# Kernel tuning notes

Measured on AMD Instinct MI355X. Metric: run time of the kernel, lower is better.

## Reference

```python
import jax, jax.numpy as jnp
import numpy as np

B, S, C, D = 128, 128, 128, 64
NQ, NT = 5000, 1441

def setup_inputs() -> dict:
    key = jax.random.key(0)
    ks = jax.random.split(key, 20)
    def xav(k, shape):
        fan_in, fan_out = shape[0], shape[1]
        lim = float(np.sqrt(6.0 / (fan_in + fan_out)))
        return jax.random.uniform(k, shape, jnp.float32, -lim, lim)
    return {
        'question_seq': jax.random.randint(ks[0], (B, S), 0, NQ),
        'correctness_seq': jax.random.randint(ks[1], (B, S), 0, 2),
        'interval_time_seq': jax.random.randint(ks[2], (B, S), 0, NT),
        'use_time_seq': jax.random.randint(ks[3], (B, S), 0, NT),
        'E_q': jax.random.normal(ks[4], (NQ, D), jnp.float32) * 0.05,
        'E_c': jax.random.normal(ks[5], (2, D), jnp.float32) * 0.05,
        'E_it': jax.random.normal(ks[6], (NT, D), jnp.float32) * 0.05,
        'E_at': jax.random.normal(ks[7], (NT, D), jnp.float32) * 0.05,
        'q_matrix': (jax.random.uniform(ks[8], (NQ, C)) < 0.1).astype(jnp.float32),
        'h0': xav(ks[9], (C, D)),
        'W1': xav(ks[10], (3 * D, D)), 'b1': jnp.zeros((D,), jnp.float32),
        'W2': xav(ks[11], (4 * D, D)), 'b2': jnp.zeros((D,), jnp.float32),
        'W3': xav(ks[12], (4 * D, D)), 'b3': jnp.zeros((D,), jnp.float32),
        'W4': xav(ks[13], (3 * D, D)), 'b4': jnp.zeros((D,), jnp.float32),
        'W5': xav(ks[14], (2 * D, D)), 'b5': jnp.zeros((D,), jnp.float32),
    }

def _lpkt_forward(question_seq, correctness_seq, interval_time_seq, use_time_seq,
                  E_q, E_c, E_it, E_at, q_matrix, h0,
                  W1, b1, W2, b2, W3, b3, W4, b4, W5, b5):
    dim_k = W1.shape[1]
    b, s = question_seq.shape
    e_emb = E_q[question_seq]            # [B,S,D]
    c_emb = E_c[correctness_seq]         # [B,S,D]
    it_emb = E_it[interval_time_seq]     # [B,S,D]
    at_emb = E_at[use_time_seq]          # [B,S,D]
    # all learning vectors (linear_1 over full sequence, as in original)
    all_learning = jnp.concatenate([e_emb, at_emb, c_emb], -1) @ W1 + b1  # [B,S,D]
    q_e_seq = q_matrix[question_seq]     # [B,S,C]

    h_pre0 = jnp.broadcast_to(h0, (b,) + h0.shape)                 # [B,C,D]
    h_tilde0 = q_e_seq[:, 0] @ h0                                  # [B,D] (h_pre is batch-replicated)
    learning0 = jnp.zeros((b, dim_k), all_learning.dtype)

    # time-major xs for t = 0 .. s-2
    xs = (jnp.swapaxes(q_e_seq[:, :-1], 0, 1),      # q_e at t
          jnp.swapaxes(q_e_seq[:, 1:], 0, 1),       # q_e at t+1
          jnp.swapaxes(it_emb[:, :-1], 0, 1),       # it at t
          jnp.swapaxes(all_learning[:, :-1], 0, 1), # learning at t
          jnp.swapaxes(e_emb[:, 1:], 0, 1))         # e embed at t+1

    def step(carry, x):
        h_pre, h_tilde_pre, learning_pre = carry
        q_e, q_e_next, it, learning, e_next = x
        x4 = jnp.concatenate([learning_pre, it, learning, h_tilde_pre], -1)   # [B,4D]
        learning_gain = jnp.tanh(x4 @ W2 + b2)
        gamma_l = jax.nn.sigmoid(x4 @ W3 + b3)
        LG = gamma_l * (learning_gain + 1.0) * 0.5                            # [B,D]
        LG_tilde = q_e[:, :, None] * LG[:, None, :]                           # [B,C,D] scatter to concepts
        c = q_e.shape[1]
        x3 = jnp.concatenate([h_pre,
                              jnp.broadcast_to(LG[:, None, :], (LG.shape[0], c, dim_k)),
                              jnp.broadcast_to(it[:, None, :], (it.shape[0], c, dim_k))], -1)
        gamma_f = jax.nn.sigmoid(x3 @ W4 + b4)                                # [B,C,D]
        h = LG_tilde + gamma_f * h_pre                                        # [B,C,D]
        h_tilde = jnp.einsum('bc,bcd->bd', q_e_next, h)                       # gather for next question
        y = jax.nn.sigmoid(jnp.concatenate([e_next, h_tilde], -1) @ W5 + b5).mean(-1)
        return (h, h_tilde, learning), y

    _, ys = jax.lax.scan(step, (h_pre0, h_tilde0, learning0), xs)  # ys: [S-1, B]
    pred = jnp.zeros((b, s), ys.dtype).at[:, 1:].set(jnp.swapaxes(ys, 0, 1))
    return pred

def reference(question_seq, correctness_seq, interval_time_seq, use_time_seq,
              E_q, E_c, E_it, E_at, q_matrix, h0,
              W1, b1, W2, b2, W3, b3, W4, b4, W5, b5):
    return _lpkt_forward(question_seq, correctness_seq, interval_time_seq, use_time_seq,
                         E_q, E_c, E_it, E_at, q_matrix, h0,
                         W1, b1, W2, b2, W3, b3, W4, b4, W5, b5)
```

## Files before the change

kernel.cpp:

```cpp
#include <hip/hip_runtime.h>
#include <hip/hip_bf16.h>


#define NB 128
#define NS 128
#define NC 128
#define ND 64
#define POS (NB*NS)

typedef __attribute__((ext_vector_type(8))) short short8;
typedef __attribute__((ext_vector_type(4))) float f32x4;
typedef __attribute__((ext_vector_type(2))) _Float16 half2_t;

__device__ __forceinline__ float rl(float v,int j){
  return __int_as_float(__builtin_amdgcn_readlane(__float_as_int(v), j));
}
__device__ __forceinline__ half2_t rlh2(half2_t v,int j){
  int x; __builtin_memcpy(&x,&v,4);
  x = __builtin_amdgcn_readlane(x,j);
  half2_t r; __builtin_memcpy(&r,&x,4); return r;
}
__device__ __forceinline__ half2_t pkrtz(float a, float b){
  auto t = __builtin_amdgcn_cvt_pkrtz(a,b);
  half2_t r; __builtin_memcpy(&r,&t,4); return r;
}
__device__ __forceinline__ float dppswap(float v){
  return __int_as_float(__builtin_amdgcn_update_dpp(0,__float_as_int(v),0xB1,0xF,0xF,true));
}
__device__ __forceinline__ float dot2h(half2_t a, half2_t b, float c){
#if __has_builtin(__builtin_amdgcn_fdot2)
  return __builtin_amdgcn_fdot2(a,b,c,false);
#else
  return fmaf((float)a[0],(float)b[0], fmaf((float)a[1],(float)b[1], c));
#endif
}

#define HBF(c, d) ((((c)<<6) + (d)) ^ (((c)&7)<<3))
#define DPP_ADD(v, CTRL) ((v) + __int_as_float(__builtin_amdgcn_update_dpp(0, __float_as_int(v), CTRL, 0xF, 0xF, true)))
#define DPP_ROWSUM(v) do { v = DPP_ADD(v,0x111); v = DPP_ADD(v,0x112); v = DPP_ADD(v,0x114); v = DPP_ADD(v,0x118); } while(0)

#define SC1 (-1.4426950408889634f)

__device__ __forceinline__ float gsig(float zp){
  return __builtin_amdgcn_rcpf(1.f + __builtin_amdgcn_exp2f(zp));
}

__global__ __launch_bounds__(64) void lpkt_pre1(
    const int* __restrict__ qseq, const int* __restrict__ cseq,
    const int* __restrict__ itseq, const int* __restrict__ atseq,
    const float* __restrict__ E_q, const float* __restrict__ E_c,
    const float* __restrict__ E_it, const float* __restrict__ E_at,
    const float* __restrict__ W1, const float* __restrict__ b1,
    const float* __restrict__ W4, const float* __restrict__ b4,
    const float* __restrict__ W5, const float* __restrict__ b5,
    float* __restrict__ AL, float* __restrict__ pre4, float* __restrict__ pre5)
{
  __shared__ float sx[4][192];
  __shared__ float sit[4][64];
  const int d = threadIdx.x;
  #pragma unroll
  for (int i = 0; i < 4; ++i) {
    int p = blockIdx.x + i*4096;
    sx[i][d]      = E_q[qseq[p]*ND + d];
    sx[i][64+d]   = E_at[atseq[p]*ND + d];
    sx[i][128+d]  = E_c[cseq[p]*ND + d];
    sit[i][d]     = E_it[itseq[p]*ND + d];
  }
  __syncthreads();
  float al[4], p4[4], p5[4];
  const float b1d = b1[d], b4d = b4[d], b5d = b5[d];
  #pragma unroll
  for (int i = 0; i < 4; ++i) { al[i] = b1d; p4[i] = b4d; p5[i] = b5d; }
  for (int k = 0; k < 192; ++k) {
    float wv = W1[k*ND + d];
    #pragma unroll
    for (int i = 0; i < 4; ++i) al[i] = fmaf(sx[i][k], wv, al[i]);
  }
  for (int k = 0; k < 64; ++k) {
    float wv4 = W4[(128+k)*ND + d];
    float wv5 = W5[k*ND + d];
    #pragma unroll
    for (int i = 0; i < 4; ++i) {
      p4[i] = fmaf(sit[i][k], wv4, p4[i]);
      p5[i] = fmaf(sx[i][k],  wv5, p5[i]);
    }
  }
  #pragma unroll
  for (int i = 0; i < 4; ++i) {
    int p = blockIdx.x + i*4096;
    AL[p*ND + d]   = al[i];
    pre4[p*ND + d] = p4[i]*SC1;
    pre5[p*ND + d] = p5[i]*SC1;
  }
}

__global__ __launch_bounds__(64) void lpkt_pre2(
    const int* __restrict__ itseq, const float* __restrict__ E_it,
    const float* __restrict__ AL,
    const float* __restrict__ W2, const float* __restrict__ b2,
    const float* __restrict__ W3, const float* __restrict__ b3,
    float* __restrict__ pre2, float* __restrict__ pre3)
{
  __shared__ float sx[4][192];
  const int d = threadIdx.x;
  int bs4[4];
  #pragma unroll
  for (int i = 0; i < 4; ++i) {
    int p = blockIdx.x + i*4064;
    int b = p / 127;
    int t = p - b*127;
    int bs = b*NS + t;
    bs4[i] = bs;
    sx[i][d]     = (t > 0) ? AL[(bs-1)*ND + d] : 0.f;
    sx[i][64+d]  = E_it[itseq[bs]*ND + d];
    sx[i][128+d] = AL[bs*ND + d];
  }
  __syncthreads();
  float a2[4], a3[4];
  const float b2d = b2[d], b3d = b3[d];
  #pragma unroll
  for (int i = 0; i < 4; ++i) { a2[i] = b2d; a3[i] = b3d; }
  for (int k = 0; k < 192; ++k) {
    float w2v = W2[k*ND + d];
    float w3v = W3[k*ND + d];
    #pragma unroll
    for (int i = 0; i < 4; ++i) {
      a2[i] = fmaf(sx[i][k], w2v, a2[i]);
      a3[i] = fmaf(sx[i][k], w3v, a3[i]);
    }
  }
  #pragma unroll
  for (int i = 0; i < 4; ++i) {
    pre2[bs4[i]*ND + d] = a2[i]*(2.f*SC1);
    pre3[bs4[i]*ND + d] = a3[i]*SC1;
  }
}

#define LOADB() do {                                                         \
  _Pragma("unroll")                                                          \
  for (int t2_=0;t2_<2;++t2_)                                                \
    _Pragma("unroll")                                                        \
    for (int k0_=0;k0_<2;++k0_)                                              \
      bfr[t2_][k0_] = *(const short8*)&sh_hbf[bfofs[t2_][k0_]];              \
} while(0)

#define MFMA8() do {                                                         \
  _Pragma("unroll")                                                          \
  for (int t2_=0;t2_<2;++t2_){                                               \
    _Pragma("unroll")                                                        \
    for (int k0_=0;k0_<2;++k0_){                                             \
      acc[0][t2_] = __builtin_amdgcn_mfma_f32_16x16x32_bf16(aW[0][k0_], bfr[t2_][k0_], acc[0][t2_],0,0,0); \
      acc[1][t2_] = __builtin_amdgcn_mfma_f32_16x16x32_bf16(aW[1][k0_], bfr[t2_][k0_], acc[1][t2_],0,0,0); \
    }                                                                        \
  }                                                                          \
} while(0)

__global__ __launch_bounds__(512)
void lpkt_seq(
    const int* __restrict__ qseq, const float* __restrict__ qmat,
    const float* __restrict__ h0,
    const float* __restrict__ W2, const float* __restrict__ W3,
    const float* __restrict__ W4, const float* __restrict__ W5,
    const float* __restrict__ pre2, const float* __restrict__ pre3,
    const float* __restrict__ pre4, const float* __restrict__ pre5,
    float* __restrict__ out)
{
  __shared__ __align__(16) unsigned short sh_hbf[NC*ND];
  __shared__ float sh_pre[32][4][64];
  __shared__ float sh_qf[32][NC];
  __shared__ float sh_htp[4][64];
  __shared__ float sh_LG[64];
  __shared__ __align__(16) unsigned sh_LGb[32];
  __shared__ float sh_out[NS];

  const int tid = threadIdx.x;
  const int w = tid>>6, l = tid&63;
  const int g = l>>4, li = l&15;
  const int b = blockIdx.x;
  const int Wq = w & 3, mm = (w>>2)*2;

  if (w==4) __builtin_amdgcn_s_setprio(1);

  short8 aW[2][2];
  #pragma unroll
  for (int mloc=0;mloc<2;++mloc)
    #pragma unroll
    for (int k0=0;k0<2;++k0){
      short8 v;
      #pragma unroll
      for (int j=0;j<8;++j){
        __hip_bfloat16 hb = __float2bfloat16(W4[(32*k0+8*g+j)*ND + 16*(mm+mloc)+li] * SC1);
        v[j] = *(short*)&hb;
      }
      aW[mloc][k0] = v;
    }
  short8 aW4b[2][2];
  #pragma unroll
  for (int mloc=0;mloc<2;++mloc)
    #pragma unroll
    for (int k0=0;k0<2;++k0){
      short8 v;
      #pragma unroll
      for (int j=0;j<8;++j){
        __hip_bfloat16 hb = __float2bfloat16(W4[(64+32*k0+8*g+j)*ND + 16*(mm+mloc)+li] * SC1);
        v[j] = *(short*)&hb;
      }
      aW4b[mloc][k0] = v;
    }

  half2_t wA[32], wB[32];
  if (w==4){
    #pragma unroll
    for (int j=0;j<32;++j){
      wA[j] = pkrtz(W2[(192+2*j)*ND + l]*(2.f*SC1), W2[(193+2*j)*ND + l]*(2.f*SC1));
      wB[j] = pkrtz(W3[(192+2*j)*ND + l]*SC1,       W3[(193+2*j)*ND + l]*SC1);
    }
  } else if (w==6){
    #pragma unroll
    for (int j=0;j<32;++j)
      wA[j] = pkrtz(W5[(64+2*j)*ND + l]*SC1, W5[(65+2*j)*ND + l]*SC1);
  }

  float hreg[2][2][4];
  int wofs[2][2], bfofs[2][2];
  #pragma unroll
  for (int mloc=0;mloc<2;++mloc)
    #pragma unroll
    for (int t2=0;t2<2;++t2){
      int c  = 32*Wq + 16*t2 + li;
      int d0 = 16*(mm+mloc) + 4*g;
      wofs[t2][mloc] = HBF(c, d0);
      float4 v = *(const float4*)&h0[c*ND + d0];
      hreg[mloc][t2][0]=v.x; hreg[mloc][t2][1]=v.y;
      hreg[mloc][t2][2]=v.z; hreg[mloc][t2][3]=v.w;
      __hip_bfloat162 c01 = __float22bfloat162_rn(make_float2(v.x,v.y));
      __hip_bfloat162 c23 = __float22bfloat162_rn(make_float2(v.z,v.w));
      uint2 pk; pk.x = *(unsigned*)&c01; pk.y = *(unsigned*)&c23;
      *(uint2*)&sh_hbf[wofs[t2][mloc]] = pk;
    }
  #pragma unroll
  for (int t2=0;t2<2;++t2)
    #pragma unroll
    for (int k0=0;k0<2;++k0)
      bfofs[t2][k0] = HBF(32*Wq+16*t2+li, 32*k0+8*g);

  #pragma unroll
  for (int k2=0;k2<2;++k2){
    int f4id = tid + k2*512;
    if (f4id < 17*32){
      int r = f4id >> 5, c4 = (f4id & 31)*4;
      int qrow = qseq[b*NS + r];
      float4 v = *(const float4*)&qmat[qrow*NC + c4];
      *(float4*)&sh_qf[r][c4] = v;
    }
  }
  #pragma unroll
  for (int k2=0;k2<2;++k2){
    int f4id = tid + k2*512;
    int u = f4id >> 6;
    int inner = f4id & 63;
    int s = inner >> 4, c4 = (inner & 15)*4;
    const float* ps = (s==0)?pre2:(s==1)?pre3:(s==2)?pre4:pre5;
    float4 v = *(const float4*)&ps[(size_t)(b*NS+u)*ND + c4];
    *(float4*)(&sh_pre[u][0][0] + inner*4) = v;
  }
  if (tid==0) sh_out[0] = 0.f;
  __syncthreads();

  {
    float part[2][4] = {{0.f,0.f,0.f,0.f},{0.f,0.f,0.f,0.f}};
    #pragma unroll
    for (int t2=0;t2<2;++t2){
      float qv = sh_qf[0][32*Wq+16*t2+li];
      #pragma unroll
      for (int mloc=0;mloc<2;++mloc)
        #pragma unroll
        for (int r2=0;r2<4;++r2)
          part[mloc][r2] = fmaf(qv, hreg[mloc][t2][r2], part[mloc][r2]);
    }
    #pragma unroll
    for (int mloc=0;mloc<2;++mloc)
      #pragma unroll
      for (int r2=0;r2<4;++r2){ float v=part[mloc][r2]; DPP_ROWSUM(v); part[mloc][r2]=v; }
    if (li==15){
      #pragma unroll
      for (int mloc=0;mloc<2;++mloc){
        float4 pv; pv.x=part[mloc][0]; pv.y=part[mloc][1]; pv.z=part[mloc][2]; pv.w=part[mloc][3];
        *(float4*)&sh_htp[Wq][16*(mm+mloc)+4*g] = pv;
      }
    }
  }
  __syncthreads();

  float qc0 = sh_qf[0][32*Wq+li];
  float qc1 = sh_qf[0][32*Wq+16+li];

  const float* prebase;
  { int s = l>>4;
    const float* ps = (s==0)?pre2:(s==1)?pre3:(s==2)?pre4:pre5;
    prebase = ps + (size_t)(b*NS)*ND + (l&15)*4; }

  for (int t=0; t<127; ++t){
    const int slot = t & 31, sn = (t+1) & 31;

    f32x4 acc[2][2];
    #pragma unroll
    for (int mloc=0;mloc<2;++mloc)
      #pragma unroll
      for (int t2=0;t2<2;++t2)
        acc[mloc][t2] = (f32x4){0.f,0.f,0.f,0.f};
    short8 bfr[2][2];

    if (w==4){
      float pv2 = sh_pre[slot][0][l], pv3 = sh_pre[slot][1][l];
      float htv = (sh_htp[0][l]+sh_htp[1][l])+(sh_htp[2][l]+sh_htp[3][l]);
      half2_t hpk = pkrtz(htv, dppswap(htv));
      float a20=pv2, a21=0.f, a30=pv3, a31=0.f;
      #pragma unroll
      for (int j=0;j<32;j+=2){
        half2_t ha = rlh2(hpk, 2*j), hb = rlh2(hpk, 2*j+2);
        a20 = dot2h(ha, wA[j],   a20); a21 = dot2h(hb, wA[j+1], a21);
        a30 = dot2h(ha, wB[j],   a30); a31 = dot2h(hb, wB[j+1], a31);
      }
      float LGl = gsig(a30+a31) * gsig(a20+a21);
      sh_LG[l] = LGl;
      float nb = dppswap(LGl);
      if (!(l&1)){
        __hip_bfloat162 pk = __float22bfloat162_rn(make_float2(LGl, nb));
        sh_LGb[l>>1] = *(unsigned*)&pk;
      }
      LOADB(); MFMA8();
    } else if (w==6){
      if (t > 0){
        float pv5 = sh_pre[slot][3][l];
        float htv = (sh_htp[0][l]+sh_htp[1][l])+(sh_htp[2][l]+sh_htp[3][l]);
        half2_t hpk = pkrtz(htv, dppswap(htv));
        float z0 = pv5, z1 = 0.f;
        #pragma unroll
        for (int j=0;j<32;j+=2){
          z0 = dot2h(rlh2(hpk, 2*j),   wA[j],   z0);
          z1 = dot2h(rlh2(hpk, 2*j+2), wA[j+1], z1);
        }
        float yv = gsig(z0+z1);
        DPP_ROWSUM(yv);
        float s = (rl(yv,15)+rl(yv,31))+(rl(yv,47)+rl(yv,63));
        if (l==0) sh_out[t] = s*(1.f/64.f);
      }
      LOADB(); MFMA8();
    } else if (w==3){
      if ((t&15)==0){
        int t0r = t+17;
        #pragma unroll
        for (int rep=0; rep<8; ++rep){
          int f4id = rep*64 + l;
          int r = t0r + (f4id>>5);
          int c4 = (f4id & 31)*4;
          if (r < NS){
            int qrow = qseq[b*NS + r];
            float4 v = *(const float4*)&qmat[qrow*NC + c4];
            *(float4*)&sh_qf[r&31][c4] = v;
          }
        }
      }
      LOADB(); MFMA8();
    } else if (w==7){
      if ((t&15)==0){
        #pragma unroll
        for (int rep=0; rep<16; ++rep){
          int u = t+16+rep;
          if (u < NS){
            float4 v = *(const float4*)&prebase[(size_t)u*ND];
            *(float4*)(&sh_pre[u&31][0][0] + l*4) = v;
          }
        }
      }
      LOADB(); MFMA8();
    } else {
      LOADB(); MFMA8();
    }
    float qn0 = sh_qf[sn][32*Wq+li];
    float qn1 = sh_qf[sn][32*Wq+16+li];
    __syncthreads();

    {
      short8 lgb[2];
      #pragma unroll
      for (int k0=0;k0<2;++k0)
        lgb[k0] = *(const short8*)((const char*)sh_LGb + 64*k0 + 16*g);
      #pragma unroll
      for (int mloc=0;mloc<2;++mloc)
        #pragma unroll
        for (int t2=0;t2<2;++t2){
          acc[mloc][t2] = __builtin_amdgcn_mfma_f32_16x16x32_bf16(aW4b[mloc][0], lgb[0], acc[mloc][t2],0,0,0);
          acc[mloc][t2] = __builtin_amdgcn_mfma_f32_16x16x32_bf16(aW4b[mloc][1], lgb[1], acc[mloc][t2],0,0,0);
        }

      float4 LG4[2]; float gi[2][4];
      #pragma unroll
      for (int mloc=0;mloc<2;++mloc){
        int d0 = 16*(mm+mloc)+4*g;
        LG4[mloc] = *(const float4*)&sh_LG[d0];
        float4 p4v = *(const float4*)&sh_pre[slot][2][d0];
        gi[mloc][0]=p4v.x; gi[mloc][1]=p4v.y; gi[mloc][2]=p4v.z; gi[mloc][3]=p4v.w;
      }
      float part[2][4] = {{0.f,0.f,0.f,0.f},{0.f,0.f,0.f,0.f}};
      #pragma unroll
      for (int t2=0;t2<2;++t2){
        float qcv = t2 ? qc1 : qc0;
        float qnv = t2 ? qn1 : qn0;
        #pragma unroll
        for (int mloc=0;mloc<2;++mloc){
          float lg4a[4] = {LG4[mloc].x, LG4[mloc].y, LG4[mloc].z, LG4[mloc].w};
          float hn[4];
          #pragma unroll
          for (int r2=0;r2<4;++r2){
            float gam = gsig(acc[mloc][t2][r2] + gi[mloc][r2]);
            hn[r2] = fmaf(qcv, lg4a[r2], gam*hreg[mloc][t2][r2]);
            hreg[mloc][t2][r2] = hn[r2];
            part[mloc][r2] = fmaf(qnv, hn[r2], part[mloc][r2]);
          }
          __hip_bfloat162 c01 = __float22bfloat162_rn(make_float2(hn[0],hn[1]));
          __hip_bfloat162 c23 = __float22bfloat162_rn(make_float2(hn[2],hn[3]));
          uint2 pk; pk.x=*(unsigned*)&c01; pk.y=*(unsigned*)&c23;
          *(uint2*)&sh_hbf[wofs[t2][mloc]] = pk;
        }
      }
      #pragma unroll
      for (int mloc=0;mloc<2;++mloc)
        #pragma unroll
        for (int r2=0;r2<4;++r2){ float v=part[mloc][r2]; DPP_ROWSUM(v); part[mloc][r2]=v; }
      if (li==15){
        #pragma unroll
        for (int mloc=0;mloc<2;++mloc){
          float4 pv; pv.x=part[mloc][0]; pv.y=part[mloc][1]; pv.z=part[mloc][2]; pv.w=part[mloc][3];
          *(float4*)&sh_htp[Wq][16*(mm+mloc)+4*g] = pv;
        }
      }
      qc0 = qn0; qc1 = qn1;
    }
    __syncthreads();
  }

  if (w==6){
    float htv = (sh_htp[0][l]+sh_htp[1][l])+(sh_htp[2][l]+sh_htp[3][l]);
    half2_t hpk = pkrtz(htv, dppswap(htv));
    float z0 = sh_pre[31][3][l], z1 = 0.f;
    #pragma unroll
    for (int j=0;j<32;j+=2){
      z0 = dot2h(rlh2(hpk, 2*j),   wA[j],   z0);
      z1 = dot2h(rlh2(hpk, 2*j+2), wA[j+1], z1);
    }
    float yv = gsig(z0+z1);
    DPP_ROWSUM(yv);
    float s = (rl(yv,15)+rl(yv,31))+(rl(yv,47)+rl(yv,63));
    if (l==0) sh_out[127] = s*(1.f/64.f);
  }
  __syncthreads();
  if (tid < NS) out[b*NS + tid] = sh_out[tid];
}

extern "C" void kernel_launch(void* const* d_in, const int* in_sizes, int n_in,
                              void* d_out, int out_size, void* d_ws, size_t ws_size,
                              hipStream_t stream)
{
  const int*   qseq  = (const int*)d_in[0];
  const int*   cseq  = (const int*)d_in[1];
  const int*   itseq = (const int*)d_in[2];
  const int*   atseq = (const int*)d_in[3];
  const float* E_q   = (const float*)d_in[4];
  const float* E_c   = (const float*)d_in[5];
  const float* E_it  = (const float*)d_in[6];
  const float* E_at  = (const float*)d_in[7];
  const float* qmat  = (const float*)d_in[8];
  const float* h0    = (const float*)d_in[9];
  const float* W1    = (const float*)d_in[10];
  const float* b1    = (const float*)d_in[11];
  const float* W2    = (const float*)d_in[12];
  const float* b2    = (const float*)d_in[13];
  const float* W3    = (const float*)d_in[14];
  const float* b3    = (const float*)d_in[15];
  const float* W4    = (const float*)d_in[16];
  const float* b4    = (const float*)d_in[17];
  const float* W5    = (const float*)d_in[18];
  const float* b5    = (const float*)d_in[19];
  float* out = (float*)d_out;

  float* wsf  = (float*)d_ws;
  float* AL   = wsf;
  float* pre2 = wsf + 1*POS*ND;
  float* pre3 = wsf + 2*POS*ND;
  float* pre4 = wsf + 3*POS*ND;
  float* pre5 = wsf + 4*POS*ND;

  lpkt_pre1<<<4096, 64, 0, stream>>>(qseq, cseq, itseq, atseq,
                                     E_q, E_c, E_it, E_at,
                                     W1, b1, W4, b4, W5, b5,
                                     AL, pre4, pre5);
  lpkt_pre2<<<4064, 64, 0, stream>>>(itseq, E_it, AL, W2, b2, W3, b3, pre2, pre3);
  lpkt_seq<<<128, 512, 0, stream>>>(qseq, qmat, h0, W2, W3, W4, W5,
                                    pre2, pre3, pre4, pre5, out);
}
```

Baseline: 273.0 us.

## Batch 16 positions per block in precompute kernels and fold gate bias into MFMA

```diff
diff --git a/kernel.cpp b/kernel.cpp
--- a/kernel.cpp
+++ b/kernel.cpp
@@ -23,6 +23,11 @@
 __device__ __forceinline__ half2_t pkrtz(float a, float b){
   auto t = __builtin_amdgcn_cvt_pkrtz(a,b);
   half2_t r; __builtin_memcpy(&r,&t,4); return r;
+}
+__device__ __forceinline__ unsigned pk_bf16(float lo, float hi){
+  unsigned r;
+  asm("v_cvt_pk_bf16_f32 %0, %1, %2" : "=v"(r) : "v"(lo), "v"(hi));
+  return r;
 }
 __device__ __forceinline__ float dppswap(float v){
   return __int_as_float(__builtin_amdgcn_update_dpp(0,__float_as_int(v),0xB1,0xF,0xF,true));
@@ -55,39 +60,40 @@
     const float* __restrict__ W5, const float* __restrict__ b5,
     float* __restrict__ AL, float* __restrict__ pre4, float* __restrict__ pre5)
 {
-  __shared__ float sx[4][192];
-  __shared__ float sit[4][64];
+  __shared__ float sx[16][192];
+  __shared__ float sit[16][64];
   const int d = threadIdx.x;
-  #pragma unroll
-  for (int i = 0; i < 4; ++i) {
-    int p = blockIdx.x + i*4096;
+  const int base = blockIdx.x * 16;
+  #pragma unroll 4
+  for (int i = 0; i < 16; ++i) {
+    int p = base + i;
     sx[i][d]      = E_q[qseq[p]*ND + d];
     sx[i][64+d]   = E_at[atseq[p]*ND + d];
     sx[i][128+d]  = E_c[cseq[p]*ND + d];
     sit[i][d]     = E_it[itseq[p]*ND + d];
   }
   __syncthreads();
-  float al[4], p4[4], p5[4];
+  float al[16], p4[16], p5[16];
   const float b1d = b1[d], b4d = b4[d], b5d = b5[d];
   #pragma unroll
-  for (int i = 0; i < 4; ++i) { al[i] = b1d; p4[i] = b4d; p5[i] = b5d; }
+  for (int i = 0; i < 16; ++i) { al[i] = b1d; p4[i] = b4d; p5[i] = b5d; }
   for (int k = 0; k < 192; ++k) {
     float wv = W1[k*ND + d];
     #pragma unroll
-    for (int i = 0; i < 4; ++i) al[i] = fmaf(sx[i][k], wv, al[i]);
+    for (int i = 0; i < 16; ++i) al[i] = fmaf(sx[i][k], wv, al[i]);
   }
   for (int k = 0; k < 64; ++k) {
     float wv4 = W4[(128+k)*ND + d];
     float wv5 = W5[k*ND + d];
     #pragma unroll
-    for (int i = 0; i < 4; ++i) {
+    for (int i = 0; i < 16; ++i) {
       p4[i] = fmaf(sit[i][k], wv4, p4[i]);
       p5[i] = fmaf(sx[i][k],  wv5, p5[i]);
     }
   }
   #pragma unroll
-  for (int i = 0; i < 4; ++i) {
-    int p = blockIdx.x + i*4096;
+  for (int i = 0; i < 16; ++i) {
+    int p = base + i;
     AL[p*ND + d]   = al[i];
     pre4[p*ND + d] = p4[i]*SC1;
     pre5[p*ND + d] = p5[i]*SC1;
@@ -101,38 +107,54 @@
     const float* __restrict__ W3, const float* __restrict__ b3,
     float* __restrict__ pre2, float* __restrict__ pre3)
 {
-  __shared__ float sx[4][192];
+  __shared__ float sal[17][64];
+  __shared__ float sit[16][64];
   const int d = threadIdx.x;
-  int bs4[4];
-  #pragma unroll
-  for (int i = 0; i < 4; ++i) {
-    int p = blockIdx.x + i*4064;
-    int b = p / 127;
-    int t = p - b*127;
-    int bs = b*NS + t;
-    bs4[i] = bs;
-    sx[i][d]     = (t > 0) ? AL[(bs-1)*ND + d] : 0.f;
-    sx[i][64+d]  = E_it[itseq[bs]*ND + d];
-    sx[i][128+d] = AL[bs*ND + d];
+  const int b = blockIdx.x >> 3;
+  const int t0 = (blockIdx.x & 7) * 16;
+  #pragma unroll 4
+  for (int i = 0; i < 17; ++i) {
+    int tt = t0 - 1 + i;
+    sal[i][d] = (tt >= 0) ? AL[(b*NS + tt)*ND + d] : 0.f;
+  }
+  #pragma unroll 4
+  for (int i = 0; i < 16; ++i) {
+    sit[i][d] = E_it[itseq[b*NS + t0 + i]*ND + d];
   }
   __syncthreads();
-  float a2[4], a3[4];
+  float a2[16], a3[16];
   const float b2d = b2[d], b3d = b3[d];
   #pragma unroll
-  for (int i = 0; i < 4; ++i) { a2[i] = b2d; a3[i] = b3d; }
-  for (int k = 0; k < 192; ++k) {
-    float w2v = W2[k*ND + d];
-    float w3v = W3[k*ND + d];
-    #pragma unroll
-    for (int i = 0; i < 4; ++i) {
-      a2[i] = fmaf(sx[i][k], w2v, a2[i]);
-      a3[i] = fmaf(sx[i][k], w3v, a3[i]);
-    }
-  }
-  #pragma unroll
-  for (int i = 0; i < 4; ++i) {
-    pre2[bs4[i]*ND + d] = a2[i]*(2.f*SC1);
-    pre3[bs4[i]*ND + d] = a3[i]*SC1;
+  for (int i = 0; i < 16; ++i) { a2[i] = b2d; a3[i] = b3d; }
+  for (int k = 0; k < 64; ++k) {
+    float w2v = W2[k*ND + d], w3v = W3[k*ND + d];
+    #pragma unroll
+    for (int i = 0; i < 16; ++i) {
+      a2[i] = fmaf(sal[i][k], w2v, a2[i]);
+      a3[i] = fmaf(sal[i][k], w3v, a3[i]);
+    }
+  }
+  for (int k = 0; k < 64; ++k) {
+    float w2v = W2[(64+k)*ND + d], w3v = W3[(64+k)*ND + d];
+    #pragma unroll
+    for (int i = 0; i < 16; ++i) {
+      a2[i] = fmaf(sit[i][k], w2v, a2[i]);
+      a3[i] = fmaf(sit[i][k], w3v, a3[i]);
+    }
+  }
+  for (int k = 0; k < 64; ++k) {
+    float w2v = W2[(128+k)*ND + d], w3v = W3[(128+k)*ND + d];
+    #pragma unroll
+    for (int i = 0; i < 16; ++i) {
+      a2[i] = fmaf(sal[i+1][k], w2v, a2[i]);
+      a3[i] = fmaf(sal[i+1][k], w3v, a3[i]);
+    }
+  }
+  #pragma unroll
+  for (int i = 0; i < 16; ++i) {
+    int p = (b*NS + t0 + i)*ND + d;
+    pre2[p] = a2[i]*(2.f*SC1);
+    pre3[p] = a3[i]*SC1;
   }
 }
 
@@ -153,6 +175,14 @@
       acc[1][t2_] = __builtin_amdgcn_mfma_f32_16x16x32_bf16(aW[1][k0_], bfr[t2_][k0_], acc[1][t2_],0,0,0); \
     }                                                                        \
   }                                                                          \
+} while(0)
+
+#define ACCINIT() do {                                                       \
+  float4 p4a_ = *(const float4*)&sh_pre[slot][2][16*mm+4*g];                 \
+  float4 p4b_ = *(const float4*)&sh_pre[slot][2][16*(mm+1)+4*g];             \
+  f32x4 ia_ = (f32x4){p4a_.x,p4a_.y,p4a_.z,p4a_.w};                          \
+  f32x4 ib_ = (f32x4){p4b_.x,p4b_.y,p4b_.z,p4b_.w};                          \
+  acc[0][0]=ia_; acc[0][1]=ia_; acc[1][0]=ib_; acc[1][1]=ib_;                \
 } while(0)
 
 __global__ __launch_bounds__(512)
@@ -233,9 +263,7 @@
       float4 v = *(const float4*)&h0[c*ND + d0];
       hreg[mloc][t2][0]=v.x; hreg[mloc][t2][1]=v.y;
       hreg[mloc][t2][2]=v.z; hreg[mloc][t2][3]=v.w;
-      __hip_bfloat162 c01 = __float22bfloat162_rn(make_float2(v.x,v.y));
-      __hip_bfloat162 c23 = __float22bfloat162_rn(make_float2(v.z,v.w));
-      uint2 pk; pk.x = *(unsigned*)&c01; pk.y = *(unsigned*)&c23;
+      uint2 pk; pk.x = pk_bf16(v.x,v.y); pk.y = pk_bf16(v.z,v.w);
       *(uint2*)&sh_hbf[wofs[t2][mloc]] = pk;
     }
   #pragma unroll
@@ -304,12 +332,8 @@
     const int slot = t & 31, sn = (t+1) & 31;
 
     f32x4 acc[2][2];
-    #pragma unroll
-    for (int mloc=0;mloc<2;++mloc)
-      #pragma unroll
-      for (int t2=0;t2<2;++t2)
-        acc[mloc][t2] = (f32x4){0.f,0.f,0.f,0.f};
     short8 bfr[2][2];
+    ACCINIT();
 
     if (w==4){
       float pv2 = sh_pre[slot][0][l], pv3 = sh_pre[slot][1][l];
@@ -325,10 +349,7 @@
       float LGl = gsig(a30+a31) * gsig(a20+a21);
       sh_LG[l] = LGl;
       float nb = dppswap(LGl);
-      if (!(l&1)){
-        __hip_bfloat162 pk = __float22bfloat162_rn(make_float2(LGl, nb));
-        sh_LGb[l>>1] = *(unsigned*)&pk;
-      }
+      if (!(l&1)) sh_LGb[l>>1] = pk_bf16(LGl, nb);
       LOADB(); MFMA8();
     } else if (w==6){
       if (t > 0){
@@ -395,14 +416,11 @@
           acc[mloc][t2] = __builtin_amdgcn_mfma_f32_16x16x32_bf16(aW4b[mloc][1], lgb[1], acc[mloc][t2],0,0,0);
         }
 
-      float4 LG4[2]; float gi[2][4];
-      #pragma unroll
-      for (int mloc=0;mloc<2;++mloc){
-        int d0 = 16*(mm+mloc)+4*g;
-        LG4[mloc] = *(const float4*)&sh_LG[d0];
-        float4 p4v = *(const float4*)&sh_pre[slot][2][d0];
-        gi[mloc][0]=p4v.x; gi[mloc][1]=p4v.y; gi[mloc][2]=p4v.z; gi[mloc][3]=p4v.w;
-      }
+      float4 LG4[2];
+      #pragma unroll
+      for (int mloc=0;mloc<2;++mloc)
+        LG4[mloc] = *(const float4*)&sh_LG[16*(mm+mloc)+4*g];
+
       float part[2][4] = {{0.f,0.f,0.f,0.f},{0.f,0.f,0.f,0.f}};
       #pragma unroll
       for (int t2=0;t2<2;++t2){
@@ -414,14 +432,12 @@
           float hn[4];
           #pragma unroll
           for (int r2=0;r2<4;++r2){
-            float gam = gsig(acc[mloc][t2][r2] + gi[mloc][r2]);
+            float gam = gsig(acc[mloc][t2][r2]);
             hn[r2] = fmaf(qcv, lg4a[r2], gam*hreg[mloc][t2][r2]);
             hreg[mloc][t2][r2] = hn[r2];
             part[mloc][r2] = fmaf(qnv, hn[r2], part[mloc][r2]);
           }
-          __hip_bfloat162 c01 = __float22bfloat162_rn(make_float2(hn[0],hn[1]));
-          __hip_bfloat162 c23 = __float22bfloat162_rn(make_float2(hn[2],hn[3]));
-          uint2 pk; pk.x=*(unsigned*)&c01; pk.y=*(unsigned*)&c23;
+          uint2 pk; pk.x = pk_bf16(hn[0],hn[1]); pk.y = pk_bf16(hn[2],hn[3]);
           *(uint2*)&sh_hbf[wofs[t2][mloc]] = pk;
         }
       }
@@ -492,11 +508,11 @@
   float* pre4 = wsf + 3*POS*ND;
   float* pre5 = wsf + 4*POS*ND;
 
-  lpkt_pre1<<<4096, 64, 0, stream>>>(qseq, cseq, itseq, atseq,
+  lpkt_pre1<<<1024, 64, 0, stream>>>(qseq, cseq, itseq, atseq,
                                      E_q, E_c, E_it, E_at,
                                      W1, b1, W4, b4, W5, b5,
                                      AL, pre4, pre5);
-  lpkt_pre2<<<4064, 64, 0, stream>>>(itseq, E_it, AL, W2, b2, W3, b3, pre2, pre3);
+  lpkt_pre2<<<1024, 64, 0, stream>>>(itseq, E_it, AL, W2, b2, W3, b3, pre2, pre3);
   lpkt_seq<<<128, 512, 0, stream>>>(qseq, qmat, h0, W2, W3, W4, W5,
                                     pre2, pre3, pre4, pre5, out);
 }
```

Measured after the change: 334.8 us. 22.6% more time.
